# Kernel optimization log

Measured on AMD Instinct MI355X. Metric: run time of the kernel, lower is better.

## Reference

```python
import jax, jax.numpy as jnp
import numpy as np

# Static conv config (matches init_kwargs)
STRIDE = (1, 1, 1)
PAD = (1, 1, 1)
DIL = (1, 1, 1)
DG = 1  # deformable groups


def setup_inputs() -> dict:
    key = jax.random.key(0)
    k1, k2, k3 = jax.random.split(key, 3)
    N, Cin, T, H, W = 2, 32, 8, 56, 56
    Cout, kT, kH, kW = 64, 3, 3, 3
    x = jax.random.normal(k1, (N, Cin, T, H, W), dtype=jnp.float32)
    # offset channels = DG * 3 * kT*kH*kW = 81 ; layout [N, dg*K*3, To, Ho, Wo]
    offset = jax.random.normal(k2, (N, DG * 3 * kT * kH * kW, T, H, W), dtype=jnp.float32)
    stdv = 1.0 / np.sqrt(Cin * kT * kH * kW)
    weight = jax.random.uniform(k3, (Cout, Cin, kT, kH, kW), dtype=jnp.float32, minval=-stdv, maxval=stdv)
    bias = jnp.zeros((Cout,), dtype=jnp.float32)
    return {"x": x, "offset": offset, "weight": weight, "bias": bias}


def _deform_conv3d(x, offset, weight, bias):
    N, C, T, H, W = x.shape
    Co, _, kT, kH, kW = weight.shape
    K = kT * kH * kW
    st, sh, sw = STRIDE
    pt_, ph_, pw_ = PAD
    dt_, dh_, dw_ = DIL
    To = (T + 2 * pt_ - (dt_ * (kT - 1) + 1)) // st + 1
    Ho = (H + 2 * ph_ - (dh_ * (kH - 1) + 1)) // sh + 1
    Wo = (W + 2 * pw_ - (dw_ * (kW - 1) + 1)) // sw + 1
    Cg = C // DG
    # offsets: [N, DG, K, 3(dt,dh,dw), To, Ho, Wo]
    off = offset.reshape(N, DG, K, 3, To, Ho, Wo)
    kt, kh, kw = [g.reshape(-1) for g in jnp.meshgrid(
        jnp.arange(kT), jnp.arange(kH), jnp.arange(kW), indexing='ij')]
    # base sampling grid per kernel tap: [K, To, Ho, Wo] via broadcasting
    bt = (jnp.arange(To) * st - pt_)[None, :, None, None] + (kt * dt_)[:, None, None, None]
    bh = (jnp.arange(Ho) * sh - ph_)[None, None, :, None] + (kh * dh_)[:, None, None, None]
    bw = (jnp.arange(Wo) * sw - pw_)[None, None, None, :] + (kw * dw_)[:, None, None, None]
    # fractional sampling positions: [N, DG, K, To, Ho, Wo]
    pt = bt[None, None] + off[:, :, :, 0]
    ph = bh[None, None] + off[:, :, :, 1]
    pw = bw[None, None] + off[:, :, :, 2]
    t0f, h0f, w0f = jnp.floor(pt), jnp.floor(ph), jnp.floor(pw)
    lt, lh, lw = pt - t0f, ph - h0f, pw - w0f
    t0 = t0f.astype(jnp.int32)
    h0 = h0f.astype(jnp.int32)
    w0 = w0f.astype(jnp.int32)
    x_flat = x.reshape(N, DG, Cg, T * H * W)
    acc = jnp.zeros((N, DG, Cg, K, To, Ho, Wo), dtype=x.dtype)
    for ct in (0, 1):
        ti = t0 + ct
        wt = lt if ct else (1.0 - lt)
        for ch in (0, 1):
            hi = h0 + ch
            wh = lh if ch else (1.0 - lh)
            for cw in (0, 1):
                wi = w0 + cw
                ww = lw if cw else (1.0 - lw)
                valid = ((ti >= 0) & (ti < T) & (hi >= 0) & (hi < H) & (wi >= 0) & (wi < W))
                idx = (jnp.clip(ti, 0, T - 1) * H + jnp.clip(hi, 0, H - 1)) * W + jnp.clip(wi, 0, W - 1)
                v = jnp.take_along_axis(x_flat, idx.reshape(N, DG, 1, -1), axis=3)
                v = v.reshape(N, DG, Cg, K, To, Ho, Wo)
                wgt = (wt * wh * ww * valid.astype(x.dtype))[:, :, None]  # [N,DG,1,K,To,Ho,Wo]
                acc = acc + v * wgt
    w_r = weight.reshape(Co, DG, Cg, K)
    out = jnp.einsum('ogck,ngcktuv->notuv', w_r, acc)
    if bias.size > 0:
        out = out + bias[None, :, None, None, None]
    return out


def reference(x, offset, weight, bias):
    return _deform_conv3d(x, offset, weight, bias)
```

## Files before the change

kernel.cpp:

```cpp
#include <hip/hip_runtime.h>
#include <hip/hip_fp16.h>

#define CIN   32
#define COUT  64
#define TT    8
#define HH    56
#define WW    56
#define KK    27
#define SP    (TT * HH * WW)
#define NB    2
#define NBLK  784
#define DBLK  1568
#define KSPLIT 14

typedef __attribute__((ext_vector_type(8))) _Float16 half8;
typedef __attribute__((ext_vector_type(4))) float    f32x4;

#define WF_OFF   0
#define XTH_OFF  (128 << 10)

__global__ __launch_bounds__(256) void prep_kernel(const float* __restrict__ x,
                                                   const float* __restrict__ w,
                                                   __half* __restrict__ xTh,
                                                   __half* __restrict__ wf) {
    const int b = blockIdx.x;
    const int t = threadIdx.x;
    if (b < NBLK) {
        __shared__ float sm[CIN][65];
        const int s0 = b * 64, n = s0 / SP, sp0 = s0 % SP;
#pragma unroll
        for (int it = 0; it < 8; ++it) {
            const int idx = it * 256 + t, c = idx >> 6, l = idx & 63;
            sm[c][l] = x[((size_t)n * CIN + c) * SP + sp0 + l];
        }
        __syncthreads();
#pragma unroll
        for (int it = 0; it < 4; ++it) {
            const int idx = it * 256 + t, l = idx >> 4, cp = idx & 15;
            ((__half2*)xTh)[((size_t)n * SP + sp0 + l) * (CIN / 2) + cp] =
                __floats2half2_rn(sm[2 * cp][l], sm[2 * cp + 1][l]);
        }
    } else {
        const int k = b - NBLK;
#pragma unroll
        for (int it = 0; it < 8; ++it) {
            const int idx  = it * 256 + t;
            const int j    = idx & 7;
            const int lane = (idx >> 3) & 63;
            const int ct   = (idx >> 9) & 3;
            const int co   = ct * 16 + (lane & 15);
            const int c    = (lane >> 4) * 8 + j;
            wf[(((size_t)k * 4 + ct) * 64 + lane) * 8 + j] =
                __float2half(w[((size_t)co * CIN + c) * KK + k]);
        }
    }
}

__global__ __launch_bounds__(256, 8) void dconv3d_kernel(const __half* __restrict__ xTh,
                                                         const float* __restrict__ off,
                                                         const __half* __restrict__ wf,
                                                         const float* __restrict__ bias,
                                                         float* __restrict__ out) {
    __shared__ __align__(16) char smem[81 * 32 * 4];
    float (*offs)[32] = reinterpret_cast<float(*)[32]>(smem);
    float (*cmb)[2][64] = reinterpret_cast<float(*)[2][64]>(smem);

    const int t    = threadIdx.x;
    const int lane = t & 63;
    const int wv   = t >> 6;
    const int wpos = wv & 1;
    const int half = wv >> 1;

    const int posI = lane >> 2;
    const int cgI  = lane & 3;
    const int jg   = lane >> 4;

    const int bp_addr = (((lane & 15) << 2) | jg) << 2;

    const int sb  = (blockIdx.x & 7) * 196 + (blockIdx.x >> 3);
    const int s0  = sb * 32;
    const int n   = s0 / SP;
    const int spb = s0 % SP;

    {
        const float* offbase = off + ((size_t)n * (3 * KK)) * SP + spb;
        for (int i = t; i < 81 * 8; i += 256) {
            const int row = i >> 3, q = i & 7;
            *(float4*)&offs[row][q * 4] = *(const float4*)(offbase + (size_t)row * SP + q * 4);
        }
    }
    __syncthreads();

    const int sp = spb + wpos * 16 + posI;
    const int to = sp / (HH * WW);
    const int hw = sp % (HH * WW);
    const int ho = hw / WW;
    const int wo = hw % WW;
    const int pl = wpos * 16 + posI;

    f32x4 acc[4];
#pragma unroll
    for (int ct = 0; ct < 4; ++ct)
#pragma unroll
        for (int r = 0; r < 4; ++r)
            acc[ct][r] = half ? 0.f : bias[ct * 16 + jg * 4 + r];

    const __half* xn = xTh + (size_t)n * SP * CIN;

    auto tap = [&](int k) {
        const int kt  = k / 9;
        const int khh = (k / 3) % 3;
        const int kww = k % 3;

        const float pt_ = (float)(to - 1 + kt)  + offs[k * 3 + 0][pl];
        const float ph_ = (float)(ho - 1 + khh) + offs[k * 3 + 1][pl];
        const float pw_ = (float)(wo - 1 + kww) + offs[k * 3 + 2][pl];

        const float ft = floorf(pt_), fh = floorf(ph_), fw = floorf(pw_);
        const float lt = pt_ - ft, lh = ph_ - fh, lw = pw_ - fw;
        const int t0 = (int)ft, h0 = (int)fh, w0 = (int)fw;
        const int t1 = t0 + 1, h1 = h0 + 1, w1 = w0 + 1;

        float awt[2], awh[2], aww[2];
        int   it2[2], ih2[2], iw2[2];
        awt[0] = ((unsigned)t0 < TT) ? (1.f - lt) : 0.f;
        awt[1] = ((unsigned)t1 < TT) ? lt : 0.f;
        it2[0] = min(max(t0, 0), TT - 1);  it2[1] = min(max(t1, 0), TT - 1);
        awh[0] = ((unsigned)h0 < HH) ? (1.f - lh) : 0.f;
        awh[1] = ((unsigned)h1 < HH) ? lh : 0.f;
        ih2[0] = min(max(h0, 0), HH - 1);  ih2[1] = min(max(h1, 0), HH - 1);
        aww[0] = ((unsigned)w0 < WW) ? (1.f - lw) : 0.f;
        aww[1] = ((unsigned)w1 < WW) ? lw : 0.f;
        iw2[0] = min(max(w0, 0), WW - 1);  iw2[1] = min(max(w1, 0), WW - 1);

        const int dT   = (it2[1] - it2[0]) * (HH * WW);
        const int dH   = (ih2[1] - ih2[0]) * WW;
        const int dW   = iw2[1] - iw2[0];
        const int base = (it2[0] * HH + ih2[0]) * WW + iw2[0];

        int   a[8];
        float cw[8];
        a[0] = base;           a[1] = base + dW;
        a[2] = base + dH;      a[3] = a[2] + dW;
        a[4] = base + dT;      a[5] = a[4] + dW;
        a[6] = a[4] + dH;      a[7] = a[6] + dW;
#pragma unroll
        for (int ci = 0; ci < 8; ++ci) {
            const int i0 = ci >> 2, i1 = (ci >> 1) & 1, i2 = ci & 1;
            cw[ci] = awt[i0] * awh[i1] * aww[i2];
        }

        float4 g[8];
#pragma unroll
        for (int ci = 0; ci < 8; ++ci)
            g[ci] = *(const float4*)(xn + (size_t)a[ci] * CIN + cgI * 8);

        __half2 vacc[4];
#pragma unroll
        for (int j = 0; j < 4; ++j) vacc[j] = __floats2half2_rn(0.f, 0.f);
#pragma unroll
        for (int ci = 0; ci < 8; ++ci) {
            const __half2* uh = (const __half2*)&g[ci];
            const __half2 cw2 = __float2half2_rn(cw[ci]);
            vacc[0] = __hfma2(cw2, uh[0], vacc[0]);
            vacc[1] = __hfma2(cw2, uh[1], vacc[1]);
            vacc[2] = __hfma2(cw2, uh[2], vacc[2]);
            vacc[3] = __hfma2(cw2, uh[3], vacc[3]);
        }

        union { __half2 h2[4]; int i[4]; half8 h8; } u, v;
#pragma unroll
        for (int d = 0; d < 4; ++d) u.h2[d] = vacc[d];
#pragma unroll
        for (int d = 0; d < 4; ++d)
            v.i[d] = __builtin_amdgcn_ds_bpermute(bp_addr, u.i[d]);
        const half8 bfrag = v.h8;

#pragma unroll
        for (int ct = 0; ct < 4; ++ct) {
            const half8 af = *(const half8*)(wf + (((size_t)k * 4 + ct) * 64 + lane) * 8);
            acc[ct] = __builtin_amdgcn_mfma_f32_16x16x32_f16(af, bfrag, acc[ct], 0, 0, 0);
        }
    };

    if (half == 0) {
#pragma unroll 2
        for (int k = 0; k < KSPLIT; ++k) tap(k);
    } else {
#pragma unroll 2
        for (int k = KSPLIT; k < KK; ++k) tap(k);
    }

    __syncthreads();
    if (half == 1) {
#pragma unroll
        for (int ct = 0; ct < 4; ++ct)
#pragma unroll
            for (int r = 0; r < 4; ++r) cmb[ct * 4 + r][wpos][lane] = acc[ct][r];
    }
    __syncthreads();
    if (half == 0) {
#pragma unroll
        for (int ct = 0; ct < 4; ++ct)
#pragma unroll
            for (int r = 0; r < 4; ++r) {
                const int co = ct * 16 + jg * 4 + r;
                out[((size_t)n * COUT + co) * SP + spb + wpos * 16 + (lane & 15)] =
                    acc[ct][r] + cmb[ct * 4 + r][wpos][lane];
            }
    }
}

extern "C" void kernel_launch(void* const* d_in, const int* in_sizes, int n_in,
                              void* d_out, int out_size, void* d_ws, size_t ws_size,
                              hipStream_t stream) {
    const float* x    = (const float*)d_in[0];
    const float* off  = (const float*)d_in[1];
    const float* w    = (const float*)d_in[2];
    const float* bias = (const float*)d_in[3];
    float* out        = (float*)d_out;

    __half* wf  = (__half*)((char*)d_ws + WF_OFF);
    __half* xTh = (__half*)((char*)d_ws + XTH_OFF);

    prep_kernel<<<NBLK + KK, 256, 0, stream>>>(x, w, xTh, wf);
    dconv3d_kernel<<<DBLK, 256, 0, stream>>>(xTh, off, wf, bias, out);
}
```

Before: 124.8 us.

## Remap lanes to MFMA B layout, drop bpermute, prefetch next-tap weights

Each lane now gathers and interpolates the channel slice that matches its MFMA B-fragment position (posI = lane&15, channel group = lane>>4). This removes the four ds_bpermute cross-lane shuffles per tap. Weight fragments for the next tap are loaded into registers before the current tap's MFMAs run, so global weight loads overlap with the gather work. The launch-bounds occupancy hint drops from 8 to 4 waves per SIMD, which frees registers for the prefetch buffers but may lower latency hiding for the scattered gathers.

```diff
diff --git a/kernel.cpp b/kernel.cpp
--- a/kernel.cpp
+++ b/kernel.cpp
@@ -56,7 +56,7 @@
     }
 }
 
-__global__ __launch_bounds__(256, 8) void dconv3d_kernel(const __half* __restrict__ xTh,
+__global__ __launch_bounds__(256, 4) void dconv3d_kernel(const __half* __restrict__ xTh,
                                                          const float* __restrict__ off,
                                                          const __half* __restrict__ wf,
                                                          const float* __restrict__ bias,
@@ -71,11 +71,8 @@
     const int wpos = wv & 1;
     const int half = wv >> 1;
 
-    const int posI = lane >> 2;
-    const int cgI  = lane & 3;
+    const int posI = lane & 15;
     const int jg   = lane >> 4;
-
-    const int bp_addr = (((lane & 15) << 2) | jg) << 2;
 
     const int sb  = (blockIdx.x & 7) * 196 + (blockIdx.x >> 3);
     const int s0  = sb * 32;
@@ -107,7 +104,20 @@
 
     const __half* xn = xTh + (size_t)n * SP * CIN;
 
-    auto tap = [&](int k) {
+    const int k0 = half ? KSPLIT : 0;
+    const int k1 = half ? KK : KSPLIT;
+
+    half8 wc0, wc1, wc2, wc3, wn0, wn1, wn2, wn3;
+    {
+        const __half* wp = wf + ((size_t)k0 * 256 + lane) * 8;
+        wc0 = *(const half8*)(wp);
+        wc1 = *(const half8*)(wp + 512);
+        wc2 = *(const half8*)(wp + 1024);
+        wc3 = *(const half8*)(wp + 1536);
+    }
+
+#pragma unroll 2
+    for (int k = k0; k < k1; ++k) {
         const int kt  = k / 9;
         const int khh = (k / 3) % 3;
         const int kww = k % 3;
@@ -153,42 +163,37 @@
         float4 g[8];
 #pragma unroll
         for (int ci = 0; ci < 8; ++ci)
-            g[ci] = *(const float4*)(xn + (size_t)a[ci] * CIN + cgI * 8);
-
-        __half2 vacc[4];
-#pragma unroll
-        for (int j = 0; j < 4; ++j) vacc[j] = __floats2half2_rn(0.f, 0.f);
+            g[ci] = *(const float4*)(xn + (size_t)a[ci] * CIN + jg * 8);
+
+        {
+            const int kn = (k + 1 < k1) ? k + 1 : k;
+            const __half* wpn = wf + ((size_t)kn * 256 + lane) * 8;
+            wn0 = *(const half8*)(wpn);
+            wn1 = *(const half8*)(wpn + 512);
+            wn2 = *(const half8*)(wpn + 1024);
+            wn3 = *(const half8*)(wpn + 1536);
+        }
+
+        union { __half2 h2[4]; half8 h8; } u;
+        u.h2[0] = __floats2half2_rn(0.f, 0.f);
+        u.h2[1] = u.h2[0]; u.h2[2] = u.h2[0]; u.h2[3] = u.h2[0];
 #pragma unroll
         for (int ci = 0; ci < 8; ++ci) {
             const __half2* uh = (const __half2*)&g[ci];
             const __half2 cw2 = __float2half2_rn(cw[ci]);
-            vacc[0] = __hfma2(cw2, uh[0], vacc[0]);
-            vacc[1] = __hfma2(cw2, uh[1], vacc[1]);
-            vacc[2] = __hfma2(cw2, uh[2], vacc[2]);
-            vacc[3] = __hfma2(cw2, uh[3], vacc[3]);
-        }
-
-        union { __half2 h2[4]; int i[4]; half8 h8; } u, v;
-#pragma unroll
-        for (int d = 0; d < 4; ++d) u.h2[d] = vacc[d];
-#pragma unroll
-        for (int d = 0; d < 4; ++d)
-            v.i[d] = __builtin_amdgcn_ds_bpermute(bp_addr, u.i[d]);
-        const half8 bfrag = v.h8;
-
-#pragma unroll
-        for (int ct = 0; ct < 4; ++ct) {
-            const half8 af = *(const half8*)(wf + (((size_t)k * 4 + ct) * 64 + lane) * 8);
-            acc[ct] = __builtin_amdgcn_mfma_f32_16x16x32_f16(af, bfrag, acc[ct], 0, 0, 0);
-        }
-    };
-
-    if (half == 0) {
-#pragma unroll 2
-        for (int k = 0; k < KSPLIT; ++k) tap(k);
-    } else {
-#pragma unroll 2
-        for (int k = KSPLIT; k < KK; ++k) tap(k);
+            u.h2[0] = __hfma2(cw2, uh[0], u.h2[0]);
+            u.h2[1] = __hfma2(cw2, uh[1], u.h2[1]);
+            u.h2[2] = __hfma2(cw2, uh[2], u.h2[2]);
+            u.h2[3] = __hfma2(cw2, uh[3], u.h2[3]);
+        }
+        const half8 bfrag = u.h8;
+
+        acc[0] = __builtin_amdgcn_mfma_f32_16x16x32_f16(wc0, bfrag, acc[0], 0, 0, 0);
+        acc[1] = __builtin_amdgcn_mfma_f32_16x16x32_f16(wc1, bfrag, acc[1], 0, 0, 0);
+        acc[2] = __builtin_amdgcn_mfma_f32_16x16x32_f16(wc2, bfrag, acc[2], 0, 0, 0);
+        acc[3] = __builtin_amdgcn_mfma_f32_16x16x32_f16(wc3, bfrag, acc[3], 0, 0, 0);
+
+        wc0 = wn0; wc1 = wn1; wc2 = wn2; wc3 = wn3;
     }
 
     __syncthreads();
@@ -205,7 +210,7 @@
 #pragma unroll
             for (int r = 0; r < 4; ++r) {
                 const int co = ct * 16 + jg * 4 + r;
-                out[((size_t)n * COUT + co) * SP + spb + wpos * 16 + (lane & 15)] =
+                out[((size_t)n * COUT + co) * SP + spb + wpos * 16 + posI] =
                     acc[ct][r] + cmb[ct * 4 + r][wpos][lane];
             }
     }
```

Result: slower. 148.0 us (+18.6%).
